# Performance work log

Hardware: AMD Instinct MI355X
Metric: run time of the kernel (lower is better)

The kernel has to match this reference:

```python
import jax, jax.numpy as jnp
import numpy as np

B, N, D, H = 64, 64, 128, 256
DIN = N + 4        # z_where(2) + one-hot(N) + actions(2)
DOUT = 2
TAU = 0.5
BN_EPS = 1e-5
KL_EPS = 1e-16


def mlp_bn(x, w1, b1, g, bb, w2, b2):
    # Linear -> ReLU -> BatchNorm1d (training mode, stats over all leading dims) -> Linear
    h = jax.nn.relu(jnp.einsum('...i,ih->...h', x, w1) + b1)
    hf = h.reshape(-1, h.shape[-1])
    mu = hf.mean(0)
    var = hf.var(0)  # biased variance, as torch BN uses for normalization
    h = (h - mu) * jax.lax.rsqrt(var + BN_EPS) * g + bb
    return jnp.einsum('...h,ho->...o', h, w2) + b2


def setup_inputs():
    key = jax.random.key(0)
    ks = jax.random.split(key, 16)
    def W(k, i, o):
        return jax.random.normal(k, (i, o), jnp.float32) / np.float32(np.sqrt(i))
    u = jax.random.uniform(ks[0], (B, N, N, 2), jnp.float32, 1e-10, 1.0 - 1e-10)
    gumbel_noise = -jnp.log(-jnp.log(u))
    z = jnp.zeros
    return {
        'states': jax.random.normal(ks[1], (B, N, D), jnp.float32),
        'z_where': jax.random.normal(ks[2], (B, N, 2), jnp.float32),
        'actions': jax.random.normal(ks[3], (B, 2), jnp.float32),
        'gumbel_noise': gumbel_noise,
        'self_w1': W(ks[4], DIN, H), 'self_b1': z((H,)), 'self_g': jnp.ones((H,)), 'self_bb': z((H,)),
        'self_w2': W(ks[5], H, D), 'self_b2': z((D,)),
        'rel_w1': W(ks[6], 2 * D, H), 'rel_b1': z((H,)), 'rel_g': jnp.ones((H,)), 'rel_bb': z((H,)),
        'rel_w2': W(ks[7], H, D), 'rel_b2': z((D,)),
        'wgt_w1': W(ks[8], 2 * D, H), 'wgt_b1': z((H,)), 'wgt_g': jnp.ones((H,)), 'wgt_bb': z((H,)),
        'wgt_w2': W(ks[9], H, 2), 'wgt_b2': z((2,)),
        'pred_w1': W(ks[10], D, H), 'pred_b1': z((H,)), 'pred_g': jnp.ones((H,)), 'pred_bb': z((H,)),
        'pred_w2': W(ks[11], H, DOUT), 'pred_b2': z((DOUT,)),
        'gru_wih': W(ks[12], 2 * D, 3 * D), 'gru_whh': W(ks[13], D, 3 * D),
        'gru_bih': z((3 * D,)), 'gru_bhh': z((3 * D,)),
    }


def prop_gt_forward(states, z_where, actions, gumbel_noise,
                    self_w1, self_b1, self_g, self_bb, self_w2, self_b2,
                    rel_w1, rel_b1, rel_g, rel_bb, rel_w2, rel_b2,
                    wgt_w1, wgt_b1, wgt_g, wgt_bb, wgt_w2, wgt_b2,
                    pred_w1, pred_b1, pred_g, pred_bb, pred_w2, pred_b2,
                    gru_wih, gru_whh, gru_bih, gru_bhh):
    b = states.shape[0]
    eye = jnp.eye(N, dtype=states.dtype)
    # feat = [z_where, one-hot id, broadcast action] : (B, N, DIN)
    z_what = jnp.broadcast_to(eye[None], (b, N, N))
    act = jnp.broadcast_to(actions[:, None, :], (b, N, 2))
    feat = jnp.concatenate([z_where, z_what, act], axis=-1)
    enc_self = mlp_bn(feat, self_w1, self_b1, self_g, self_bb, self_w2, self_b2)  # (B,N,D)

    # recurrent dynamics: pairwise state concat (B, N, N, 2D)
    s_self = jnp.broadcast_to(states[:, :, None, :], (b, N, N, D))
    s_other = jnp.broadcast_to(states[:, None, :, :], (b, N, N, D))
    feat_matrix = jnp.concatenate([s_self, s_other], axis=-1)

    relational = mlp_bn(feat_matrix, rel_w1, rel_b1, rel_g, rel_bb, rel_w2, rel_b2)  # (B,N,N,D)
    logits = mlp_bn(feat_matrix, wgt_w1, wgt_b1, wgt_g, wgt_bb, wgt_w2, wgt_b2)      # (B,N,N,2)

    # gumbel-softmax, hard with straight-through
    y_soft = jax.nn.softmax((logits + gumbel_noise) / TAU, axis=-1)
    y_hard = jax.nn.one_hot(jnp.argmax(y_soft, axis=-1), 2, dtype=y_soft.dtype)
    y = jax.lax.stop_gradient(y_hard - y_soft) + y_soft
    weight = y[..., 0:1]  # (B,N,N,1)

    # KL(prob || prior) as in NRI
    log_prior = jnp.log(jnp.array([0.05, 0.95], dtype=logits.dtype))
    prob = jax.nn.softmax(logits, axis=-1)
    kl_loss = jnp.sum(prob * (jnp.log(prob + KL_EPS) - log_prior)) / (N * b)

    # self mask: zero diagonal edges
    weight = weight * (1.0 - eye)[None, :, :, None]

    enc_rel = jnp.sum(weight * relational, axis=2)  # (B,N,D)

    # TrackerRNN: GRU cell update of states with [enc_self, enc_rel]
    x = jnp.concatenate([enc_self, enc_rel], axis=-1)  # (B,N,2D)
    gi = jnp.einsum('bni,ih->bnh', x, gru_wih) + gru_bih
    gh = jnp.einsum('bnd,dh->bnh', states, gru_whh) + gru_bhh
    gi_r, gi_z, gi_n = jnp.split(gi, 3, axis=-1)
    gh_r, gh_z, gh_n = jnp.split(gh, 3, axis=-1)
    r = jax.nn.sigmoid(gi_r + gh_r)
    zg = jax.nn.sigmoid(gi_z + gh_z)
    n = jnp.tanh(gi_n + r * gh_n)
    updated_state = (1.0 - zg) * n + zg * states  # (B,N,D)

    z_where_next = mlp_bn(updated_state, pred_w1, pred_b1, pred_g, pred_bb, pred_w2, pred_b2)
    return (updated_state, z_where_next.reshape(b, -1), weight, kl_loss)


def reference(states, z_where, actions, gumbel_noise,
              self_w1, self_b1, self_g, self_bb, self_w2, self_b2,
              rel_w1, rel_b1, rel_g, rel_bb, rel_w2, rel_b2,
              wgt_w1, wgt_b1, wgt_g, wgt_bb, wgt_w2, wgt_b2,
              pred_w1, pred_b1, pred_g, pred_bb, pred_w2, pred_b2,
              gru_wih, gru_whh, gru_bih, gru_bhh):
    return prop_gt_forward(states, z_where, actions, gumbel_noise,
                           self_w1, self_b1, self_g, self_bb, self_w2, self_b2,
                           rel_w1, rel_b1, rel_g, rel_bb, rel_w2, rel_b2,
                           wgt_w1, wgt_b1, wgt_g, wgt_bb, wgt_w2, wgt_b2,
                           pred_w1, pred_b1, pred_g, pred_bb, pred_w2, pred_b2,
                           gru_wih, gru_whh, gru_bih, gru_bhh)
```

## Files before the change

### kernel.cpp

```cpp
#include <hip/hip_runtime.h>
#include <math.h>

#define BATCH 64
#define NOBJ  64
#define DDIM  128
#define HDIM  256
#define ROWS  (BATCH*NOBJ)
#define PAIRS (ROWS*NOBJ)

#define OFF_A_REL    (0ull)
#define OFF_B_REL    (4ull<<20)
#define OFF_A_WGT    (8ull<<20)
#define OFF_B_WGT    (12ull<<20)
#define OFF_BWT      (16ull<<20)
#define OFF_H_SELF   (20ull<<20)
#define OFF_ENC_SELF (24ull<<20)
#define OFF_ENC_REL  (26ull<<20)
#define OFF_H_PRED   (28ull<<20)
#define OFF_STATS    (32ull<<20)
#define OFF_KLP      (OFF_STATS + 16384)
#define OFF_W2P      (OFF_STATS + 65536)
#define OFF_C2       (OFF_W2P + 128*1024)
#define OFF_W2PD     (OFF_C2 + 512)
#define OFF_C2W      (OFF_W2PD + 4096)
#define OFF_SW2P     (OFF_C2W + 256)
#define OFF_SC2      (OFF_SW2P + 128*1024)

#define OUT_UPD 0
#define OUT_ZWN (ROWS*DDIM)
#define OUT_WGT (OUT_ZWN + ROWS*2)
#define OUT_KL  (OUT_WGT + PAIRS)

__global__ __launch_bounds__(256) void k_pre(
    const float* __restrict__ states,
    const float* __restrict__ rel_w1, const float* __restrict__ rel_b1,
    const float* __restrict__ wgt_w1, const float* __restrict__ wgt_b1,
    const float* __restrict__ z_where, const float* __restrict__ actions,
    const float* __restrict__ self_w1, const float* __restrict__ self_b1,
    float* __restrict__ A_rel, float* __restrict__ B_rel,
    float* __restrict__ A_wgt, float* __restrict__ B_wgt,
    float* __restrict__ B_wgtT, float* __restrict__ h_self,
    double* __restrict__ stats)
{
    const int t = threadIdx.x;
    const int view = blockIdx.y;
    const int row0 = blockIdx.x * 16;

    if (view == 4) {
        const float w_zw0 = self_w1[0*256+t], w_zw1 = self_w1[1*256+t];
        const float w_a0  = self_w1[66*256+t], w_a1 = self_w1[67*256+t];
        const float bb1 = self_b1[t];
        double sum = 0.0, ssq = 0.0;
        for (int r = 0; r < 16; ++r) {
            const int row = row0 + r;
            const int b = row >> 6, i = row & 63;
            const float zw0 = z_where[row*2], zw1 = z_where[row*2+1];
            const float a0 = actions[b*2], a1 = actions[b*2+1];
            float v = self_w1[(2+i)*256+t] + bb1;
            v = fmaf(zw0, w_zw0, v); v = fmaf(zw1, w_zw1, v);
            v = fmaf(a0, w_a0, v);   v = fmaf(a1, w_a1, v);
            v = fmaxf(v, 0.f);
            h_self[row*256+t] = v;
            sum += (double)v; ssq = fma((double)v, (double)v, ssq);
        }
        atomicAdd(&stats[4*256+t], sum);
        atomicAdd(&stats[5*256+t], ssq);
        return;
    }

    __shared__ float s_tile[16][128];
    for (int f4 = t; f4 < 512; f4 += 256)
        *(float4*)&s_tile[0][f4*4] = *(const float4*)&states[row0*128 + f4*4];
    __syncthreads();

    const float* wbase = (view == 0) ? rel_w1
                       : (view == 1) ? rel_w1 + 128*256
                       : (view == 2) ? wgt_w1
                       :               wgt_w1 + 128*256;
    const float* wp = wbase + t;
    float acc[16];
#pragma unroll
    for (int r = 0; r < 16; ++r) acc[r] = 0.f;
#pragma unroll 4
    for (int k = 0; k < 128; ++k) {
        const float wv = wp[k*256];
#pragma unroll
        for (int r = 0; r < 16; ++r) acc[r] = fmaf(s_tile[r][k], wv, acc[r]);
    }

    if (view == 0) {
        const float bias = rel_b1[t];
#pragma unroll
        for (int r = 0; r < 16; ++r) A_rel[(row0+r)*256 + t] = acc[r] + bias;
    } else if (view == 1) {
#pragma unroll
        for (int r = 0; r < 16; ++r) B_rel[(row0+r)*256 + t] = acc[r];
    } else if (view == 2) {
        const float bias = wgt_b1[t];
#pragma unroll
        for (int r = 0; r < 16; ++r) A_wgt[(row0+r)*256 + t] = acc[r] + bias;
    } else {
#pragma unroll
        for (int r = 0; r < 16; ++r) B_wgt[(row0+r)*256 + t] = acc[r];
        const int b = row0 >> 6, j0 = row0 & 63;
        float* bt = &B_wgtT[((size_t)b*256 + t)*64 + j0];
        *(float4*)(bt+0)  = make_float4(acc[0],  acc[1],  acc[2],  acc[3]);
        *(float4*)(bt+4)  = make_float4(acc[4],  acc[5],  acc[6],  acc[7]);
        *(float4*)(bt+8)  = make_float4(acc[8],  acc[9],  acc[10], acc[11]);
        *(float4*)(bt+12) = make_float4(acc[12], acc[13], acc[14], acc[15]);
    }
}

__global__ __launch_bounds__(256) void k_bn_stats(
    const float* __restrict__ A_rel, const float* __restrict__ B_rel,
    const float* __restrict__ A_wgt, const float* __restrict__ B_wgt,
    double* __restrict__ stats)
{
    const int h = threadIdx.x;
    const int b = blockIdx.y, i0 = blockIdx.x * 8;
    float ar[8], aw[8];
#pragma unroll
    for (int r = 0; r < 8; ++r) {
        ar[r] = A_rel[(b*64 + i0 + r)*256 + h];
        aw[r] = A_wgt[(b*64 + i0 + r)*256 + h];
    }
    float  srel0 = 0.f, ssrel0 = 0.f, srel1 = 0.f, ssrel1 = 0.f;
    double swgt = 0.0, sswgt = 0.0;
    for (int j = 0; j < 64; j += 2) {
        const float br0 = B_rel[(b*64+j)*256 + h];
        const float bw0 = B_wgt[(b*64+j)*256 + h];
        const float br1 = B_rel[(b*64+j+1)*256 + h];
        const float bw1 = B_wgt[(b*64+j+1)*256 + h];
#pragma unroll
        for (int r = 0; r < 8; ++r) {
            const float v0 = fmaxf(ar[r] + br0, 0.f);
            srel0 += v0; ssrel0 = fmaf(v0, v0, ssrel0);
            const float vw0 = fmaxf(aw[r] + bw0, 0.f);
            swgt += (double)vw0; sswgt = fma((double)vw0, (double)vw0, sswgt);
        }
#pragma unroll
        for (int r = 0; r < 8; ++r) {
            const float v1 = fmaxf(ar[r] + br1, 0.f);
            srel1 += v1; ssrel1 = fmaf(v1, v1, ssrel1);
            const float vw1 = fmaxf(aw[r] + bw1, 0.f);
            swgt += (double)vw1; sswgt = fma((double)vw1, (double)vw1, sswgt);
        }
    }
    atomicAdd(&stats[0*256+h], (double)(srel0 + srel1));
    atomicAdd(&stats[1*256+h], (double)(ssrel0 + ssrel1));
    atomicAdd(&stats[2*256+h], swgt);
    atomicAdd(&stats[3*256+h], sswgt);
}

__global__ __launch_bounds__(256) void k_finalize(
    const double* __restrict__ stats,
    const float* __restrict__ rel_g, const float* __restrict__ rel_bb,
    const float* __restrict__ rel_w2, const float* __restrict__ rel_b2,
    const float* __restrict__ wgt_g, const float* __restrict__ wgt_bb,
    const float* __restrict__ wgt_w2, const float* __restrict__ wgt_b2,
    const float* __restrict__ self_g, const float* __restrict__ self_bb,
    const float* __restrict__ self_w2, const float* __restrict__ self_b2,
    float* __restrict__ W2p, float* __restrict__ c2,
    double* __restrict__ W2pd, double* __restrict__ c2w,
    float* __restrict__ sW2p, float* __restrict__ sc2)
{
    __shared__ float  rscale[256], rshift[256], sscale[256], sshift[256];
    __shared__ double wshift[256];
    const int k = threadIdx.x;
    {
        const double cnt = 262144.0;
        double mu  = stats[0*256+k]/cnt;
        double var = stats[1*256+k]/cnt - mu*mu;
        float  sc  = (float)((double)rel_g[k] / sqrt(var + 1e-5));
        rscale[k] = sc;
        rshift[k] = rel_bb[k] - (float)mu * sc;
        double muw  = stats[2*256+k]/cnt;
        double varw = stats[3*256+k]/cnt - muw*muw;
        double scw  = (double)wgt_g[k] / sqrt(varw + 1e-5);
        wshift[k]   = (double)wgt_bb[k] - muw*scw;
        if (blockIdx.x == 0) {
            W2pd[2*k]   = scw * (double)wgt_w2[2*k];
            W2pd[2*k+1] = scw * (double)wgt_w2[2*k+1];
        }
        const double cnts = 4096.0;
        double mus  = stats[4*256+k]/cnts;
        double vars = stats[5*256+k]/cnts - mus*mus;
        float  scs  = (float)((double)self_g[k] / sqrt(vars + 1e-5));
        sscale[k] = scs;
        sshift[k] = self_bb[k] - (float)mus*scs;
    }
    __syncthreads();
    const int base = blockIdx.x * 8192;
    for (int idx = base + k; idx < base + 8192; idx += 256) {
        const int kk = idx >> 7;
        W2p[idx]  = rscale[kk]*rel_w2[idx];
        sW2p[idx] = sscale[kk]*self_w2[idx];
    }
    if (blockIdx.x == 0) {
        if (k < 128) {
            float acc = rel_b2[k], accs = self_b2[k];
            for (int kk = 0; kk < 256; ++kk) {
                acc  = fmaf(rshift[kk], rel_w2[kk*128+k], acc);
                accs = fmaf(sshift[kk], self_w2[kk*128+k], accs);
            }
            c2[k] = acc; sc2[k] = accs;
        }
        if (k < 2) {
            double acc = (double)wgt_b2[k];
            for (int kk = 0; kk < 256; ++kk) acc += wshift[kk]*(double)wgt_w2[kk*2+k];
            c2w[k] = acc;
        }
    }
}

__global__ __launch_bounds__(256) void k_main(
    const float* __restrict__ A_rel, const float* __restrict__ B_rel,
    const float* __restrict__ A_wgt, const float* __restrict__ B_wgtT,
    const double* __restrict__ W2pd, const double* __restrict__ c2w,
    const float* __restrict__ gumbel,
    const float* __restrict__ W2p, const float* __restrict__ c2,
    float* __restrict__ enc_rel, float* __restrict__ weight_out,
    float* __restrict__ klp)
{
    __shared__ float  a_lds[4][256];
    __shared__ double w2_lds[512];
    __shared__ double red0[4][4][64], red1[4][4][64];
    __shared__ float  w_lds[4][64];
    __shared__ float  klred[256];
    __shared__ float  h_lds[4][256];
    __shared__ float  redf[4][256];
    const int t = threadIdx.x;
    const int blk = blockIdx.x;
    const int row0 = blk * 4;
    const int b = row0 >> 6;

    w2_lds[t]     = W2pd[t];
    w2_lds[256+t] = W2pd[256+t];
    float a_rel[4];
#pragma unroll
    for (int r = 0; r < 4; ++r) {
        a_lds[r][t] = A_wgt[(row0+r)*256 + t];
        a_rel[r]    = A_rel[(row0+r)*256 + t];
    }
    __syncthreads();

    {
        const int j = t & 63, q = t >> 6;
        double acc0[4] = {0,0,0,0}, acc1[4] = {0,0,0,0};
        const float* btp = &B_wgtT[((size_t)b*256 + q*64)*64 + j];
#pragma unroll 4
        for (int kk = 0; kk < 64; ++kk) {
            const int k = q*64 + kk;
            const float  bw = btp[kk*64];
            const double w0 = w2_lds[2*k], w1 = w2_lds[2*k+1];
#pragma unroll
            for (int r = 0; r < 4; ++r) {
                const double hw = (double)fmaxf(a_lds[r][k] + bw, 0.f);
                acc0[r] = fma(hw, w0, acc0[r]);
                acc1[r] = fma(hw, w1, acc1[r]);
            }
        }
#pragma unroll
        for (int r = 0; r < 4; ++r) { red0[r][q][j] = acc0[r]; red1[r][q][j] = acc1[r]; }
    }
    __syncthreads();

    {
        const int r = t >> 6, j = t & 63;
        const double l0 = red0[r][0][j]+red0[r][1][j]+red0[r][2][j]+red0[r][3][j] + c2w[0];
        const double l1 = red1[r][0][j]+red1[r][1][j]+red1[r][2][j]+red1[r][3][j] + c2w[1];
        const int row = row0 + r;
        const float g0 = gumbel[(row*64+j)*2], g1 = gumbel[(row*64+j)*2+1];
        float w = (l0 + (double)g0 >= l1 + (double)g1) ? 1.f : 0.f;
        if (j == (row & 63)) w = 0.f;
        w_lds[r][j] = w;
        weight_out[row*64 + j] = w;
        const float lf0 = (float)l0, lf1 = (float)l1;
        const float m = fmaxf(lf0, lf1);
        const float e0 = expf(lf0 - m), e1 = expf(lf1 - m);
        const float s = e0 + e1;
        const float p0 = e0/s, p1 = e1/s;
        const float lp0 = -2.9957323f;
        const float lp1 = -0.05129329f;
        klred[t] = p0*(logf(p0+1e-16f) - lp0) + p1*(logf(p1+1e-16f) - lp1);
    }
    __syncthreads();
    if (t < 64) {
        float s = klred[t] + klred[t+64] + klred[t+128] + klred[t+192];
        for (int off = 32; off; off >>= 1) s += __shfl_down(s, off);
        if (t == 0) klp[blk] = s;
    }

    float sumw[4] = {0,0,0,0};
    {
        float g[4] = {0,0,0,0};
#pragma unroll 4
        for (int j = 0; j < 64; ++j) {
            const float br = B_rel[(b*64+j)*256 + t];
#pragma unroll
            for (int r = 0; r < 4; ++r) {
                const float w = w_lds[r][j];
                sumw[r] += w;
                g[r] = fmaf(w, fmaxf(a_rel[r] + br, 0.f), g[r]);
            }
        }
#pragma unroll
        for (int r = 0; r < 4; ++r) h_lds[r][t] = g[r];
    }
    __syncthreads();
    {
        const int d = t & 127, half = t >> 7;
        float acc[4] = {0,0,0,0};
        const float* wp = &W2p[half*128*128 + d];
#pragma unroll 2
        for (int kk = 0; kk < 128; ++kk) {
            const float wv = wp[kk*128];
#pragma unroll
            for (int r = 0; r < 4; ++r)
                acc[r] = fmaf(h_lds[r][half*128 + kk], wv, acc[r]);
        }
#pragma unroll
        for (int r = 0; r < 4; ++r) redf[r][t] = acc[r];
    }
    __syncthreads();
    if (t < 128) {
#pragma unroll
        for (int r = 0; r < 4; ++r)
            enc_rel[(row0+r)*128 + t] = redf[r][t] + redf[r][t+128] + sumw[r]*c2[t];
    }
}

__global__ __launch_bounds__(256) void k_enc_self(
    const float* __restrict__ h_self, const float* __restrict__ sW2p,
    const float* __restrict__ sc2, float* __restrict__ enc_self)
{
    __shared__ float h_lds[16*256];
    const int t = threadIdx.x;
    const int row0 = blockIdx.x * 16;
    for (int f4 = t; f4 < 1024; f4 += 256)
        *(float4*)&h_lds[f4*4] = *(const float4*)&h_self[row0*256 + f4*4];
    __syncthreads();
    const int d = t & 127, half = t >> 7;
    float acc[16];
#pragma unroll
    for (int r = 0; r < 16; ++r) acc[r] = 0.f;
    for (int kk = 0; kk < 128; ++kk) {
        const int k = half*128 + kk;
        const float wv = sW2p[k*128 + d];
#pragma unroll
        for (int r = 0; r < 16; ++r) acc[r] = fmaf(h_lds[r*256 + k], wv, acc[r]);
    }
    __syncthreads();
#pragma unroll
    for (int r = 0; r < 16; ++r) h_lds[r*256 + t] = acc[r];
    __syncthreads();
    for (int idx = t; idx < 16*128; idx += 256) {
        const int r = idx >> 7, dd = idx & 127;
        enc_self[(row0+r)*128 + dd] = h_lds[r*256 + dd] + h_lds[r*256 + 128 + dd] + sc2[dd];
    }
}

__global__ __launch_bounds__(384) void k_gru(
    const float* __restrict__ enc_self, const float* __restrict__ enc_rel,
    const float* __restrict__ states,
    const float* __restrict__ wih, const float* __restrict__ whh,
    const float* __restrict__ bih, const float* __restrict__ bhh,
    float* __restrict__ updated)
{
    __shared__ float x_lds[4][256];
    __shared__ float s_lds[4][128];
    __shared__ float gi_lds[4][384];
    __shared__ float gh_lds[4][384];
    const int t = threadIdx.x;
    const int row0 = blockIdx.x * 4;
    for (int idx = t; idx < 4*256; idx += 384) {
        const int r = idx >> 8, k = idx & 255;
        x_lds[r][k] = (k < 128) ? enc_self[(row0+r)*128 + k]
                                : enc_rel[(row0+r)*128 + (k-128)];
    }
    for (int idx = t; idx < 4*128; idx += 384) {
        const int r = idx >> 7, k = idx & 127;
        s_lds[r][k] = states[(row0+r)*128 + k];
    }
    __syncthreads();
    float gi[4], gh[4];
    const float bi = bih[t], bh = bhh[t];
#pragma unroll
    for (int r = 0; r < 4; ++r) { gi[r] = bi; gh[r] = bh; }
#pragma unroll 4
    for (int k = 0; k < 128; ++k) {
        const float wi_ = wih[k*384 + t];
        const float wh_ = whh[k*384 + t];
#pragma unroll
        for (int r = 0; r < 4; ++r) {
            gi[r] = fmaf(x_lds[r][k], wi_, gi[r]);
            gh[r] = fmaf(s_lds[r][k], wh_, gh[r]);
        }
    }
#pragma unroll 4
    for (int k = 128; k < 256; ++k) {
        const float wi_ = wih[k*384 + t];
#pragma unroll
        for (int r = 0; r < 4; ++r) gi[r] = fmaf(x_lds[r][k], wi_, gi[r]);
    }
#pragma unroll
    for (int r = 0; r < 4; ++r) { gi_lds[r][t] = gi[r]; gh_lds[r][t] = gh[r]; }
    __syncthreads();
    for (int idx = t; idx < 4*128; idx += 384) {
        const int r = idx >> 7, d = idx & 127;
        const float gr = gi_lds[r][d]       + gh_lds[r][d];
        const float gz = gi_lds[r][128+d]   + gh_lds[r][128+d];
        const float rr = 1.f/(1.f + expf(-gr));
        const float zz = 1.f/(1.f + expf(-gz));
        const float nn = tanhf(gi_lds[r][256+d] + rr*gh_lds[r][256+d]);
        updated[(row0+r)*128 + d] = (1.f - zz)*nn + zz*s_lds[r][d];
    }
}

__global__ __launch_bounds__(256) void k_pred_h(
    const float* __restrict__ updated, const float* __restrict__ w1,
    const float* __restrict__ b1, float* __restrict__ h_pred,
    double* __restrict__ stats)
{
    __shared__ float u_lds[16][128];
    const int h = threadIdx.x;
    const int row0 = blockIdx.x * 16;
    for (int f4 = h; f4 < 512; f4 += 256)
        *(float4*)&u_lds[0][f4*4] = *(const float4*)&updated[row0*128 + f4*4];
    __syncthreads();
    float acc[16];
    const float bb1 = b1[h];
#pragma unroll
    for (int r = 0; r < 16; ++r) acc[r] = bb1;
#pragma unroll 4
    for (int k = 0; k < 128; ++k) {
        const float w = w1[k*256 + h];
#pragma unroll
        for (int r = 0; r < 16; ++r) acc[r] = fmaf(u_lds[r][k], w, acc[r]);
    }
    double sum = 0.0, ssq = 0.0;
#pragma unroll
    for (int r = 0; r < 16; ++r) {
        const float v = fmaxf(acc[r], 0.f);
        h_pred[(row0+r)*256 + h] = v;
        sum += (double)v; ssq = fma((double)v, (double)v, ssq);
    }
    atomicAdd(&stats[6*256+h], sum);
    atomicAdd(&stats[7*256+h], ssq);
}

__global__ __launch_bounds__(256) void k_pred_out(
    const float* __restrict__ h_pred, const double* __restrict__ stats,
    const float* __restrict__ g, const float* __restrict__ bbv,
    const float* __restrict__ w2, const float* __restrict__ b2,
    const float* __restrict__ klp,
    float* __restrict__ out_zw, float* __restrict__ out_kl)
{
    __shared__ float scale_lds[256], shift_lds[256];
    __shared__ float h_lds[32*256];
    __shared__ float red0[256], red1[256];
    __shared__ double kred[4];
    const int t = threadIdx.x;
    {
        const double mu  = stats[6*256+t]/4096.0;
        const double var = stats[7*256+t]/4096.0 - mu*mu;
        const float  sc  = (float)((double)g[t]/sqrt(var + 1e-5));
        scale_lds[t] = sc;
        shift_lds[t] = bbv[t] - (float)mu*sc;
    }
    const int row0 = blockIdx.x * 32;
    for (int idx = t; idx < 32*256; idx += 256)
        h_lds[idx] = h_pred[row0*256 + idx];
    __syncthreads();
    const int rl = t >> 3, q = t & 7;
    float a0 = 0.f, a1 = 0.f;
    for (int kk = 0; kk < 32; ++kk) {
        const int k = q*32 + kk;
        const float hn = fmaf(h_lds[rl*256 + k], scale_lds[k], shift_lds[k]);
        a0 = fmaf(hn, w2[k*2],   a0);
        a1 = fmaf(hn, w2[k*2+1], a1);
    }
    red0[t] = a0; red1[t] = a1;
    __syncthreads();
    if (t < 32) {
        float z0 = b2[0], z1 = b2[1];
        for (int q2 = 0; q2 < 8; ++q2) { z0 += red0[t*8+q2]; z1 += red1[t*8+q2]; }
        out_zw[(row0+t)*2]   = z0;
        out_zw[(row0+t)*2+1] = z1;
    }
    if (blockIdx.x == 0) {
        double s = 0.0;
        for (int idx = t; idx < 1024; idx += 256) s += (double)klp[idx];
        for (int off = 32; off; off >>= 1) s += __shfl_down(s, off);
        if ((t & 63) == 0) kred[t >> 6] = s;
        __syncthreads();
        if (t == 0)
            out_kl[0] = (float)((kred[0]+kred[1]+kred[2]+kred[3]) / 4096.0);
    }
}

extern "C" void kernel_launch(void* const* d_in, const int* in_sizes, int n_in,
                              void* d_out, int out_size, void* d_ws, size_t ws_size,
                              hipStream_t stream) {
    const float* states   = (const float*)d_in[0];
    const float* z_where  = (const float*)d_in[1];
    const float* actions  = (const float*)d_in[2];
    const float* gumbel   = (const float*)d_in[3];
    const float* self_w1  = (const float*)d_in[4];
    const float* self_b1  = (const float*)d_in[5];
    const float* self_g   = (const float*)d_in[6];
    const float* self_bb  = (const float*)d_in[7];
    const float* self_w2  = (const float*)d_in[8];
    const float* self_b2  = (const float*)d_in[9];
    const float* rel_w1   = (const float*)d_in[10];
    const float* rel_b1   = (const float*)d_in[11];
    const float* rel_g    = (const float*)d_in[12];
    const float* rel_bb   = (const float*)d_in[13];
    const float* rel_w2   = (const float*)d_in[14];
    const float* rel_b2   = (const float*)d_in[15];
    const float* wgt_w1   = (const float*)d_in[16];
    const float* wgt_b1   = (const float*)d_in[17];
    const float* wgt_g    = (const float*)d_in[18];
    const float* wgt_bb   = (const float*)d_in[19];
    const float* wgt_w2   = (const float*)d_in[20];
    const float* wgt_b2   = (const float*)d_in[21];
    const float* pred_w1  = (const float*)d_in[22];
    const float* pred_b1  = (const float*)d_in[23];
    const float* pred_g   = (const float*)d_in[24];
    const float* pred_bb  = (const float*)d_in[25];
    const float* pred_w2  = (const float*)d_in[26];
    const float* pred_b2  = (const float*)d_in[27];
    const float* gru_wih  = (const float*)d_in[28];
    const float* gru_whh  = (const float*)d_in[29];
    const float* gru_bih  = (const float*)d_in[30];
    const float* gru_bhh  = (const float*)d_in[31];

    char* ws = (char*)d_ws;
    float*  A_rel  = (float*) (ws + OFF_A_REL);
    float*  B_rel  = (float*) (ws + OFF_B_REL);
    float*  A_wgt  = (float*) (ws + OFF_A_WGT);
    float*  B_wgt  = (float*) (ws + OFF_B_WGT);
    float*  B_wgtT = (float*) (ws + OFF_BWT);
    float*  h_self = (float*) (ws + OFF_H_SELF);
    float*  encS   = (float*) (ws + OFF_ENC_SELF);
    float*  encR   = (float*) (ws + OFF_ENC_REL);
    float*  h_pred = (float*) (ws + OFF_H_PRED);
    double* stats  = (double*)(ws + OFF_STATS);
    float*  klp    = (float*) (ws + OFF_KLP);
    float*  W2p    = (float*) (ws + OFF_W2P);
    float*  c2     = (float*) (ws + OFF_C2);
    double* W2pd   = (double*)(ws + OFF_W2PD);
    double* c2w    = (double*)(ws + OFF_C2W);
    float*  sW2p   = (float*) (ws + OFF_SW2P);
    float*  sc2    = (float*) (ws + OFF_SC2);

    float* out = (float*)d_out;

    hipMemsetAsync(ws + OFF_STATS, 0, 8*256*8, stream);

    k_pre<<<dim3(256, 5), 256, 0, stream>>>(states, rel_w1, rel_b1, wgt_w1, wgt_b1,
                                            z_where, actions, self_w1, self_b1,
                                            A_rel, B_rel, A_wgt, B_wgt, B_wgtT,
                                            h_self, stats);
    k_bn_stats<<<dim3(8, 64), 256, 0, stream>>>(A_rel, B_rel, A_wgt, B_wgt, stats);
    k_finalize<<<4, 256, 0, stream>>>(stats, rel_g, rel_bb, rel_w2, rel_b2,
                                      wgt_g, wgt_bb, wgt_w2, wgt_b2,
                                      self_g, self_bb, self_w2, self_b2,
                                      W2p, c2, W2pd, c2w, sW2p, sc2);
    k_main<<<1024, 256, 0, stream>>>(A_rel, B_rel, A_wgt, B_wgtT, W2pd, c2w,
                                     gumbel, W2p, c2, encR, out + OUT_WGT, klp);
    k_enc_self<<<256, 256, 0, stream>>>(h_self, sW2p, sc2, encS);
    k_gru<<<1024, 384, 0, stream>>>(encS, encR, states, gru_wih, gru_whh,
                                    gru_bih, gru_bhh, out + OUT_UPD);
    k_pred_h<<<256, 256, 0, stream>>>(out + OUT_UPD, pred_w1, pred_b1, h_pred, stats);
    k_pred_out<<<128, 256, 0, stream>>>(h_pred, stats, pred_g, pred_bb, pred_w2, pred_b2,
                                        klp, out + OUT_ZWN, out + OUT_KL);
}
```

Baseline: 200.0 us.

## Merge k_pre views, give GRU threads two columns, zero stats via kernel

```diff
diff --git a/kernel.cpp b/kernel.cpp
--- a/kernel.cpp
+++ b/kernel.cpp
@@ -31,6 +31,11 @@
 #define OUT_WGT (OUT_ZWN + ROWS*2)
 #define OUT_KL  (OUT_WGT + PAIRS)
 
+__global__ __launch_bounds__(256) void k_zero(double* __restrict__ p)
+{
+    p[blockIdx.x*256 + threadIdx.x] = 0.0;
+}
+
 __global__ __launch_bounds__(256) void k_pre(
     const float* __restrict__ states,
     const float* __restrict__ rel_w1, const float* __restrict__ rel_b1,
@@ -46,7 +51,7 @@
     const int view = blockIdx.y;
     const int row0 = blockIdx.x * 16;
 
-    if (view == 4) {
+    if (view == 2) {
         const float w_zw0 = self_w1[0*256+t], w_zw1 = self_w1[1*256+t];
         const float w_a0  = self_w1[66*256+t], w_a1 = self_w1[67*256+t];
         const float bb1 = self_b1[t];
@@ -73,41 +78,44 @@
         *(float4*)&s_tile[0][f4*4] = *(const float4*)&states[row0*128 + f4*4];
     __syncthreads();
 
-    const float* wbase = (view == 0) ? rel_w1
-                       : (view == 1) ? rel_w1 + 128*256
-                       : (view == 2) ? wgt_w1
-                       :               wgt_w1 + 128*256;
-    const float* wp = wbase + t;
-    float acc[16];
-#pragma unroll
-    for (int r = 0; r < 16; ++r) acc[r] = 0.f;
+    const float* wbase = (view == 0) ? rel_w1 : wgt_w1;
+    const float* wpA = wbase + t;
+    const float* wpB = wbase + 128*256 + t;
+    float accA[16], accB[16];
+#pragma unroll
+    for (int r = 0; r < 16; ++r) { accA[r] = 0.f; accB[r] = 0.f; }
 #pragma unroll 4
     for (int k = 0; k < 128; ++k) {
-        const float wv = wp[k*256];
-#pragma unroll
-        for (int r = 0; r < 16; ++r) acc[r] = fmaf(s_tile[r][k], wv, acc[r]);
+        const float wvA = wpA[k*256];
+        const float wvB = wpB[k*256];
+#pragma unroll
+        for (int r = 0; r < 16; ++r) {
+            const float s = s_tile[r][k];
+            accA[r] = fmaf(s, wvA, accA[r]);
+            accB[r] = fmaf(s, wvB, accB[r]);
+        }
     }
 
     if (view == 0) {
         const float bias = rel_b1[t];
 #pragma unroll
-        for (int r = 0; r < 16; ++r) A_rel[(row0+r)*256 + t] = acc[r] + bias;
-    } else if (view == 1) {
-#pragma unroll
-        for (int r = 0; r < 16; ++r) B_rel[(row0+r)*256 + t] = acc[r];
-    } else if (view == 2) {
+        for (int r = 0; r < 16; ++r) {
+            A_rel[(row0+r)*256 + t] = accA[r] + bias;
+            B_rel[(row0+r)*256 + t] = accB[r];
+        }
+    } else {
         const float bias = wgt_b1[t];
 #pragma unroll
-        for (int r = 0; r < 16; ++r) A_wgt[(row0+r)*256 + t] = acc[r] + bias;
-    } else {
-#pragma unroll
-        for (int r = 0; r < 16; ++r) B_wgt[(row0+r)*256 + t] = acc[r];
+        for (int r = 0; r < 16; ++r) {
+            A_wgt[(row0+r)*256 + t] = accA[r] + bias;
+            B_wgt[(row0+r)*256 + t] = accB[r];
+        }
         const int b = row0 >> 6, j0 = row0 & 63;
         float* bt = &B_wgtT[((size_t)b*256 + t)*64 + j0];
-        *(float4*)(bt+0)  = make_float4(acc[0],  acc[1],  acc[2],  acc[3]);
-        *(float4*)(bt+4)  = make_float4(acc[4],  acc[5],  acc[6],  acc[7]);
-        *(float4*)(bt+8)  = make_float4(acc[8],  acc[9],  acc[10], acc[11]);
-        *(float4*)(bt+12) = make_float4(acc[12], acc[13], acc[14], acc[15]);
+        *(float4*)(bt+0)  = make_float4(accB[0],  accB[1],  accB[2],  accB[3]);
+        *(float4*)(bt+4)  = make_float4(accB[4],  accB[5],  accB[6],  accB[7]);
+        *(float4*)(bt+8)  = make_float4(accB[8],  accB[9],  accB[10], accB[11]);
+        *(float4*)(bt+12) = make_float4(accB[12], accB[13], accB[14], accB[15]);
     }
 }
 
@@ -360,7 +368,7 @@
     }
 }
 
-__global__ __launch_bounds__(384) void k_gru(
+__global__ __launch_bounds__(192) void k_gru(
     const float* __restrict__ enc_self, const float* __restrict__ enc_rel,
     const float* __restrict__ states,
     const float* __restrict__ wih, const float* __restrict__ whh,
@@ -373,40 +381,79 @@
     __shared__ float gh_lds[4][384];
     const int t = threadIdx.x;
     const int row0 = blockIdx.x * 4;
-    for (int idx = t; idx < 4*256; idx += 384) {
+    for (int idx = t; idx < 4*256; idx += 192) {
         const int r = idx >> 8, k = idx & 255;
         x_lds[r][k] = (k < 128) ? enc_self[(row0+r)*128 + k]
                                 : enc_rel[(row0+r)*128 + (k-128)];
     }
-    for (int idx = t; idx < 4*128; idx += 384) {
+    for (int idx = t; idx < 4*128; idx += 192) {
         const int r = idx >> 7, k = idx & 127;
         s_lds[r][k] = states[(row0+r)*128 + k];
     }
     __syncthreads();
-    float gi[4], gh[4];
-    const float bi = bih[t], bh = bhh[t];
-#pragma unroll
-    for (int r = 0; r < 4; ++r) { gi[r] = bi; gh[r] = bh; }
-#pragma unroll 4
-    for (int k = 0; k < 128; ++k) {
-        const float wi_ = wih[k*384 + t];
-        const float wh_ = whh[k*384 + t];
+    const int c0 = t, c1 = t + 192;
+    float gi0[4], gh0[4], gi1[4], gh1[4];
+    const float bi0 = bih[c0], bh0 = bhh[c0];
+    const float bi1 = bih[c1], bh1 = bhh[c1];
+#pragma unroll
+    for (int r = 0; r < 4; ++r) { gi0[r] = bi0; gh0[r] = bh0; gi1[r] = bi1; gh1[r] = bh1; }
+
+    for (int k0 = 0; k0 < 128; k0 += 4) {
+        float4 xv[4], sv[4];
 #pragma unroll
         for (int r = 0; r < 4; ++r) {
-            gi[r] = fmaf(x_lds[r][k], wi_, gi[r]);
-            gh[r] = fmaf(s_lds[r][k], wh_, gh[r]);
-        }
-    }
-#pragma unroll 4
-    for (int k = 128; k < 256; ++k) {
-        const float wi_ = wih[k*384 + t];
-#pragma unroll
-        for (int r = 0; r < 4; ++r) gi[r] = fmaf(x_lds[r][k], wi_, gi[r]);
-    }
-#pragma unroll
-    for (int r = 0; r < 4; ++r) { gi_lds[r][t] = gi[r]; gh_lds[r][t] = gh[r]; }
-    __syncthreads();
-    for (int idx = t; idx < 4*128; idx += 384) {
+            xv[r] = *(const float4*)&x_lds[r][k0];
+            sv[r] = *(const float4*)&s_lds[r][k0];
+        }
+        float wi0[4], wi1[4], wh0[4], wh1[4];
+#pragma unroll
+        for (int kk = 0; kk < 4; ++kk) {
+            wi0[kk] = wih[(k0+kk)*384 + c0];
+            wi1[kk] = wih[(k0+kk)*384 + c1];
+            wh0[kk] = whh[(k0+kk)*384 + c0];
+            wh1[kk] = whh[(k0+kk)*384 + c1];
+        }
+#pragma unroll
+        for (int kk = 0; kk < 4; ++kk) {
+#pragma unroll
+            for (int r = 0; r < 4; ++r) {
+                const float x = ((const float*)&xv[r])[kk];
+                const float s = ((const float*)&sv[r])[kk];
+                gi0[r] = fmaf(x, wi0[kk], gi0[r]);
+                gi1[r] = fmaf(x, wi1[kk], gi1[r]);
+                gh0[r] = fmaf(s, wh0[kk], gh0[r]);
+                gh1[r] = fmaf(s, wh1[kk], gh1[r]);
+            }
+        }
+    }
+    for (int k0 = 128; k0 < 256; k0 += 4) {
+        float4 xv[4];
+#pragma unroll
+        for (int r = 0; r < 4; ++r)
+            xv[r] = *(const float4*)&x_lds[r][k0];
+        float wi0[4], wi1[4];
+#pragma unroll
+        for (int kk = 0; kk < 4; ++kk) {
+            wi0[kk] = wih[(k0+kk)*384 + c0];
+            wi1[kk] = wih[(k0+kk)*384 + c1];
+        }
+#pragma unroll
+        for (int kk = 0; kk < 4; ++kk) {
+#pragma unroll
+            for (int r = 0; r < 4; ++r) {
+                const float x = ((const float*)&xv[r])[kk];
+                gi0[r] = fmaf(x, wi0[kk], gi0[r]);
+                gi1[r] = fmaf(x, wi1[kk], gi1[r]);
+            }
+        }
+    }
+#pragma unroll
+    for (int r = 0; r < 4; ++r) {
+        gi_lds[r][c0] = gi0[r]; gi_lds[r][c1] = gi1[r];
+        gh_lds[r][c0] = gh0[r]; gh_lds[r][c1] = gh1[r];
+    }
+    __syncthreads();
+    for (int idx = t; idx < 4*128; idx += 192) {
         const int r = idx >> 7, d = idx & 127;
         const float gr = gi_lds[r][d]       + gh_lds[r][d];
         const float gz = gi_lds[r][128+d]   + gh_lds[r][128+d];
@@ -556,9 +603,8 @@
 
     float* out = (float*)d_out;
 
-    hipMemsetAsync(ws + OFF_STATS, 0, 8*256*8, stream);
-
-    k_pre<<<dim3(256, 5), 256, 0, stream>>>(states, rel_w1, rel_b1, wgt_w1, wgt_b1,
+    k_zero<<<8, 256, 0, stream>>>(stats);
+    k_pre<<<dim3(256, 3), 256, 0, stream>>>(states, rel_w1, rel_b1, wgt_w1, wgt_b1,
                                             z_where, actions, self_w1, self_b1,
                                             A_rel, B_rel, A_wgt, B_wgt, B_wgtT,
                                             h_self, stats);
@@ -570,7 +616,7 @@
     k_main<<<1024, 256, 0, stream>>>(A_rel, B_rel, A_wgt, B_wgtT, W2pd, c2w,
                                      gumbel, W2p, c2, encR, out + OUT_WGT, klp);
     k_enc_self<<<256, 256, 0, stream>>>(h_self, sW2p, sc2, encS);
-    k_gru<<<1024, 384, 0, stream>>>(encS, encR, states, gru_wih, gru_whh,
+    k_gru<<<1024, 192, 0, stream>>>(encS, encR, states, gru_wih, gru_whh,
                                     gru_bih, gru_bhh, out + OUT_UPD);
     k_pred_h<<<256, 256, 0, stream>>>(out + OUT_UPD, pred_w1, pred_b1, h_pred, stats);
     k_pred_out<<<128, 256, 0, stream>>>(h_pred, stats, pred_g, pred_bb, pred_w2, pred_b2,
```

After: 202.3 us. Within noise of the previous version (+1.1%).
